# Kernel optimization log

Measured on AMD Instinct MI355X. Metric: run time of the kernel, lower is better.

## Reference

```python
import jax, jax.numpy as jnp
import numpy as np

B, T, D, H, K, V, L = 512, 80, 540, 6, 90, 30522, 6  # batch, ctx, d_model, heads, head_size, vocab, blocks


def _layernorm(x, g, b, eps=1e-5):
    m = jnp.mean(x, axis=-1, keepdims=True)
    v = jnp.mean(jnp.square(x - m), axis=-1, keepdims=True)
    return (x - m) * jax.lax.rsqrt(v + eps) * g + b


def setup_inputs() -> dict:
    key = jax.random.key(0)
    ks = jax.random.split(key, 12)
    s = 0.02
    return {
        "x_batch": jax.random.randint(ks[0], (B, T), 0, V),
        "embed": jax.random.normal(ks[1], (V, D), jnp.float32) * s,
        "pos_embed": jax.random.normal(ks[2], (T, D), jnp.float32) * s,
        # per-block stacked per-head projection weights, applied as x @ W
        "Wq": jax.random.normal(ks[3], (L, H, D, K), jnp.float32) * s,
        "Wk": jax.random.normal(ks[4], (L, H, D, K), jnp.float32) * s,
        "Wv": jax.random.normal(ks[5], (L, H, D, K), jnp.float32) * s,
        "W1": jax.random.normal(ks[6], (L, D, H * K), jnp.float32) * s,
        "b1": jnp.zeros((L, H * K), jnp.float32),
        "W2": jax.random.normal(ks[7], (L, H * K, D), jnp.float32) * s,
        "b2": jnp.zeros((L, D), jnp.float32),
        "ln1_g": jnp.ones((L, D), jnp.float32),
        "ln1_b": jnp.zeros((L, D), jnp.float32),
        "ln2_g": jnp.ones((L, D), jnp.float32),
        "ln2_b": jnp.zeros((L, D), jnp.float32),
        "Wc": jax.random.normal(ks[8], (T * D, 1), jnp.float32) * s,
        "bc": jnp.zeros((1,), jnp.float32),
    }


def reference(x_batch, embed, pos_embed, Wq, Wk, Wv, W1, b1, W2, b2,
              ln1_g, ln1_b, ln2_g, ln2_b, Wc, bc):
    x = embed[x_batch] + pos_embed[jnp.arange(x_batch.shape[1])]  # [B,T,D]
    scale = K ** -0.5
    for i in range(L):
        q = jnp.einsum('btd,hdk->bhtk', x, Wq[i])
        k = jnp.einsum('btd,hdk->bhtk', x, Wk[i])
        v = jnp.einsum('btd,hdk->bhtk', x, Wv[i])
        scores = jnp.einsum('btk,bsk->bts'.replace('b', 'bh'), q, k) * scale  # [B,H,T,T]
        # original: Softmax(dim=1) on [B,T,T] -> normalize over the QUERY axis
        attn = jax.nn.softmax(scores, axis=2)
        o = jnp.einsum('bhts,bhsk->bhtk', attn, v)
        o = o.transpose(0, 2, 1, 3).reshape(x.shape)  # concat heads -> [B,T,D]
        x = _layernorm(o + x, ln1_g[i], ln1_b[i])
        ff = jax.nn.relu(x @ W1[i] + b1[i]) @ W2[i] + b2[i]
        x = _layernorm(ff + x, ln2_g[i], ln2_b[i])
    flat = x.reshape(x.shape[0], -1)  # [B, T*D]
    return flat @ Wc + bc  # [B,1]
```

## Files before the change

kernel.cpp:

```cpp
#include <hip/hip_runtime.h>
#include <hip/hip_bf16.h>
#include <math.h>

typedef __hip_bfloat16 bf16;
typedef __bf16 bf16x8 __attribute__((ext_vector_type(8)));
typedef __bf16 bf16x4 __attribute__((ext_vector_type(4)));
typedef float floatx4 __attribute__((ext_vector_type(4)));

#define BB 512
#define TT 80
#define DD 540
#define HH 6
#define KK 90
#define LL 6
#define HK 540
#define KKA 96
#define HKA 576
#define NQA 1728
#define BT 40960
#define TD 43200
#define KP2 576
#define NQ2 1792
#define NF 640
#define NF2 768
#define TP 104
#define NKT2 18
#define BUFSZ 12288

__device__ inline float toF(bf16 x) { return __bfloat162float(x); }


__global__ void prep_wqkv(const float* __restrict__ Wq,
                          const float* __restrict__ Wk,
                          const float* __restrict__ Wv,
                          bf16* __restrict__ wTt) {
    int idx = blockIdx.x * blockDim.x + threadIdx.x;
    const int total = LL * NQ2 * KP2;
    if (idx >= total) return;
    int k = idx % KP2;
    int n = (idx / KP2) % NQ2;
    int l = idx / (KP2 * NQ2);
    float v = 0.f;
    if (k < DD && n < NQA) {
        int sel = n / HKA;
        int nn = n - sel * HKA;
        int h = nn / KKA, kk = nn - h * KKA;
        if (kk < KK) {
            const float* W = (sel == 0) ? Wq : ((sel == 1) ? Wk : Wv);
            v = W[(((size_t)l * HH + h) * DD + k) * KK + kk];
        }
    }
    wTt[idx] = __float2bfloat16(v);
}

__global__ void prep_wt(const float* __restrict__ W, bf16* __restrict__ Wt) {
    int idx = blockIdx.x * blockDim.x + threadIdx.x;
    const int total = LL * NF2 * KP2;
    if (idx >= total) return;
    int k = idx % KP2;
    int n = (idx / KP2) % NF2;
    int l = idx / (KP2 * NF2);
    float v = 0.f;
    if (k < DD && n < DD)
        v = W[((size_t)l * DD + k) * DD + n];
    Wt[idx] = __float2bfloat16(v);
}

__global__ void embed_kernel(const int* __restrict__ ids,
                             const float* __restrict__ embed,
                             const float* __restrict__ pos,
                             bf16* __restrict__ xc, int rows) {
    int idx = blockIdx.x * blockDim.x + threadIdx.x;
    int total = rows * KP2;
    if (idx >= total) return;
    int d = idx % KP2;
    int bt = idx / KP2;
    float v = 0.f;
    if (d < DD) {
        int t = bt % TT;
        v = embed[(size_t)ids[bt] * DD + d] + pos[t * DD + d];
    }
    xc[idx] = __float2bfloat16(v);
}


__device__ inline void stage3(const bf16* __restrict__ Ab, int lda,
                              const bf16* __restrict__ Bb,
                              bf16* ldsbuf, int k0, int tid) {
#pragma unroll
    for (int i = 0; i < 3; ++i) {
        int s = tid + i * 512;
        int isB = (s >= 512) ? 1 : 0;
        int s2 = s - isB * 512;
        int row = s2 >> 2, c = s2 & 3;
        int cs = c ^ ((row >> 1) & 3);
        const bf16* src = isB ? (Bb + (size_t)row * KP2 + k0 + cs * 8)
                              : (Ab + (size_t)row * lda + k0 + cs * 8);
        bf16* dst = ldsbuf + isB * 4096 + s2 * 8;
        __builtin_amdgcn_global_load_lds(
            (const __attribute__((address_space(1))) void*)src,
            (__attribute__((address_space(3))) void*)dst, 16, 0, 0);
    }
}

__global__ __launch_bounds__(512, 4) void mfma_gemm2(
    const bf16* __restrict__ A, int lda,
    const bf16* __restrict__ Bt,
    bf16* __restrict__ C, int ldc, int Nreal,
    const float* __restrict__ bias, int relu)
{
    extern __shared__ __align__(16) bf16 ldsb[];
    const int tid = threadIdx.x;
    const int lane = tid & 63;
    const int wave = tid >> 6;
    const int wr = wave >> 2;
    const int wc = wave & 3;
    const int q = lane >> 4, r = lane & 15;

    int bx = blockIdx.x, by = blockIdx.y;
    {
        int nwg = gridDim.x * gridDim.y;
        if ((nwg & 7) == 0) {
            int orig = by * gridDim.x + bx;
            int per = nwg >> 3;
            int swz = (orig & 7) * per + (orig >> 3);
            bx = swz % gridDim.x;
            by = swz / gridDim.x;
        }
    }
    const int row0 = by * 128;
    const int col0 = bx * 256;

    floatx4 acc[4][4];
#pragma unroll
    for (int i = 0; i < 4; ++i)
#pragma unroll
        for (int j = 0; j < 4; ++j) acc[i][j] = (floatx4){0.f, 0.f, 0.f, 0.f};

    const bf16* Ab = A + (size_t)row0 * lda;
    const bf16* Bb = Bt + (size_t)col0 * KP2;

    const int ksw = (q ^ ((r >> 1) & 3)) * 8;

    stage3(Ab, lda, Bb, ldsb, 0, tid);
    asm volatile("s_waitcnt vmcnt(0)" ::: "memory");
    __builtin_amdgcn_sched_barrier(0);
    __builtin_amdgcn_s_barrier();
    __builtin_amdgcn_sched_barrier(0);

    for (int kt = 0; kt < NKT2; ++kt) {
        bf16* buf  = ldsb + (kt & 1) * BUFSZ;
        bf16* sbuf = ldsb + ((kt + 1) & 1) * BUFSZ;

        if (kt + 1 < NKT2)
            stage3(Ab, lda, Bb, sbuf, (kt + 1) * 32, tid);

        bf16x8 a0[4], b0[4];
#pragma unroll
        for (int i = 0; i < 4; ++i) {
            int row_ = wr * 64 + i * 16 + r;
            a0[i] = *(const bf16x8*)(buf + row_ * 32 + ksw);
        }
#pragma unroll
        for (int j = 0; j < 4; ++j) {
            int row_ = wc * 64 + j * 16 + r;
            b0[j] = *(const bf16x8*)(buf + 4096 + row_ * 32 + ksw);
        }

        __builtin_amdgcn_s_setprio(1);
#pragma unroll
        for (int i = 0; i < 4; ++i)
#pragma unroll
            for (int j = 0; j < 4; ++j)
                acc[i][j] = __builtin_amdgcn_mfma_f32_16x16x32_bf16(
                    a0[i], b0[j], acc[i][j], 0, 0, 0);
        __builtin_amdgcn_s_setprio(0);

        asm volatile("s_waitcnt vmcnt(0)" ::: "memory");
        __builtin_amdgcn_sched_barrier(0);
        __builtin_amdgcn_s_barrier();
        __builtin_amdgcn_sched_barrier(0);
    }

#pragma unroll
    for (int mi = 0; mi < 4; ++mi) {
        int m0 = row0 + wr * 64 + mi * 16 + q * 4;
#pragma unroll
        for (int ni = 0; ni < 4; ++ni) {
            int n = col0 + wc * 64 + ni * 16 + r;
            if (n < ldc) {
                bool valid = (n < Nreal);
                float bv = (valid && bias) ? bias[n] : 0.f;
#pragma unroll
                for (int reg = 0; reg < 4; ++reg) {
                    float v = acc[mi][ni][reg] + bv;
                    if (relu) v = fmaxf(v, 0.f);
                    if (!valid) v = 0.f;
                    C[(size_t)(m0 + reg) * ldc + n] = __float2bfloat16(v);
                }
            }
        }
    }
}

__global__ __launch_bounds__(320) void attn_mfma(const bf16* __restrict__ qkv,
                                                 bf16* __restrict__ obuf) {
    extern __shared__ bf16 lds[];
    bf16* Qs = lds;
    bf16* Ks = lds + 80 * TP;
    bf16* Vt = lds + 160 * TP;
    __bf16* Vtb = (__bf16*)Vt;
    const int b = blockIdx.x / HH, h = blockIdx.x % HH;
    const int tid = threadIdx.x;
    const int lane = tid & 63;
    const int w = tid >> 6;
    const int q = lane >> 4, r = lane & 15;
    const bf16* base = qkv + (size_t)b * TT * NQA + h * KKA;

    for (int i = tid; i < TT * 12; i += 320) {
        int t = i / 12, kg = i % 12;
        const bf16* qr2 = base + (size_t)t * NQA + kg * 8;
        bf16x8 qv = *(const bf16x8*)qr2;
        bf16x8 kv2 = *(const bf16x8*)(qr2 + HKA);
        bf16x8 vv = *(const bf16x8*)(qr2 + 2 * HKA);
        *(bf16x8*)(Qs + t * TP + kg * 8) = qv;
        *(bf16x8*)(Ks + t * TP + kg * 8) = kv2;
#pragma unroll
        for (int j = 0; j < 8; ++j)
            Vtb[(kg * 8 + j) * TP + t] = vv[j];
    }
    for (int i = tid; i < 96 * 2; i += 320) {
        int kv = i >> 1, sg = i & 1;
        *(bf16x8*)(Vt + kv * TP + 80 + sg * 8) = (bf16x8)(__bf16)0.0f;
    }
    __syncthreads();

    floatx4 acc[5];
#pragma unroll
    for (int i = 0; i < 5; ++i) acc[i] = (floatx4){0.f, 0.f, 0.f, 0.f};
    bf16x8 bf[3];
#pragma unroll
    for (int ks = 0; ks < 3; ++ks)
        bf[ks] = *(const bf16x8*)(Ks + (16 * w + r) * TP + ks * 32 + q * 8);
#pragma unroll
    for (int ti = 0; ti < 5; ++ti) {
#pragma unroll
        for (int ks = 0; ks < 3; ++ks) {
            bf16x8 af = *(const bf16x8*)(Qs + (16 * ti + r) * TP + ks * 32 + q * 8);
            acc[ti] = __builtin_amdgcn_mfma_f32_16x16x32_bf16(af, bf[ks], acc[ti], 0, 0, 0);
        }
    }

    const float scale = 0.105409255338946f;
    float m = -1e30f;
#pragma unroll
    for (int ti = 0; ti < 5; ++ti)
#pragma unroll
        for (int reg = 0; reg < 4; ++reg) {
            acc[ti][reg] *= scale;
            m = fmaxf(m, acc[ti][reg]);
        }
    m = fmaxf(m, __shfl_xor(m, 16));
    m = fmaxf(m, __shfl_xor(m, 32));
    float sum = 0.f;
    float e[5][4];
#pragma unroll
    for (int ti = 0; ti < 5; ++ti)
#pragma unroll
        for (int reg = 0; reg < 4; ++reg) {
            e[ti][reg] = __expf(acc[ti][reg] - m);
            sum += e[ti][reg];
        }
    sum += __shfl_xor(sum, 16);
    sum += __shfl_xor(sum, 32);
    float inv = 1.f / sum;

    __syncthreads();

    bf16* P = Ks;
#pragma unroll
    for (int ti = 0; ti < 5; ++ti)
#pragma unroll
        for (int reg = 0; reg < 4; ++reg)
            P[(16 * ti + q * 4 + reg) * TP + 16 * w + r] =
                __float2bfloat16(e[ti][reg] * inv);
    for (int i = tid; i < TT * 2; i += 320) {
        int t2 = i >> 1, sg = i & 1;
        *(bf16x8*)(P + t2 * TP + 80 + sg * 8) = (bf16x8)(__bf16)0.0f;
    }
    __syncthreads();

    bf16x8 af2[3];
#pragma unroll
    for (int ks = 0; ks < 3; ++ks)
        af2[ks] = *(const bf16x8*)(P + (16 * w + r) * TP + ks * 32 + q * 8);
    bf16* ob = obuf + ((size_t)b * TT) * NF + h * KK;
#pragma unroll
    for (int nt = 0; nt < 6; ++nt) {
        floatx4 o = (floatx4){0.f, 0.f, 0.f, 0.f};
#pragma unroll
        for (int ks = 0; ks < 3; ++ks) {
            bf16x8 bv = *(const bf16x8*)(Vt + (16 * nt + r) * TP + ks * 32 + q * 8);
            o = __builtin_amdgcn_mfma_f32_16x16x32_bf16(af2[ks], bv, o, 0, 0, 0);
        }
        int kv = 16 * nt + r;
        if (kv < KK) {
#pragma unroll
            for (int reg = 0; reg < 4; ++reg) {
                int t2 = 16 * w + q * 4 + reg;
                ob[(size_t)t2 * NF + kv] = __float2bfloat16(o[reg]);
            }
        }
    }
}

__global__ __launch_bounds__(256) void add_ln_kernel(const bf16* __restrict__ delta,
                                                     bf16* __restrict__ x,
                                                     const float* __restrict__ g,
                                                     const float* __restrict__ bta,
                                                     int nrows) {
    const int w = threadIdx.x >> 6;
    const int lane = threadIdx.x & 63;
    const int row = blockIdx.x * 4 + w;
    if (row >= nrows) return;
    const bf16* dr = delta + (size_t)row * NF;
    bf16* xr = x + (size_t)row * KP2;

    float v[3][4];
    float s1 = 0.f, s2 = 0.f;
#pragma unroll
    for (int s = 0; s < 3; ++s) {
        int c = s * 256 + lane * 4;
        if (c < DD) {
            bf16x4 dv = *(const bf16x4*)(dr + c);
            bf16x4 xv = *(const bf16x4*)(xr + c);
#pragma unroll
            for (int j = 0; j < 4; ++j) {
                float t = (float)dv[j] + (float)xv[j];
                v[s][j] = t;
                s1 += t; s2 += t * t;
            }
        } else {
#pragma unroll
            for (int j = 0; j < 4; ++j) v[s][j] = 0.f;
        }
    }
#pragma unroll
    for (int o = 32; o > 0; o >>= 1) {
        s1 += __shfl_xor(s1, o, 64);
        s2 += __shfl_xor(s2, o, 64);
    }
    const float mean = s1 * (1.f / DD);
    const float var = s2 * (1.f / DD) - mean * mean;
    const float rstd = rsqrtf(var + 1e-5f);
#pragma unroll
    for (int s = 0; s < 3; ++s) {
        int c = s * 256 + lane * 4;
        if (c < DD) {
            float4 gv = *(const float4*)(g + c);
            float4 bv = *(const float4*)(bta + c);
            bf16x4 ov;
            ov[0] = (__bf16)((v[s][0] - mean) * rstd * gv.x + bv.x);
            ov[1] = (__bf16)((v[s][1] - mean) * rstd * gv.y + bv.y);
            ov[2] = (__bf16)((v[s][2] - mean) * rstd * gv.z + bv.z);
            ov[3] = (__bf16)((v[s][3] - mean) * rstd * gv.w + bv.w);
            *(bf16x4*)(xr + c) = ov;
        }
    }
}

__global__ __launch_bounds__(256) void final_kernel(const bf16* __restrict__ xc,
                                                    const float* __restrict__ Wc,
                                                    const float* __restrict__ bc,
                                                    float* __restrict__ out) {
    int b = blockIdx.x;
    int tid = threadIdx.x;
    const bf16* xb = xc + (size_t)b * TT * KP2;
    float s = 0.f;
    for (int i = tid; i < TD; i += 256) {
        int t = i / DD, d = i - t * DD;
        s += toF(xb[(size_t)t * KP2 + d]) * Wc[i];
    }
    for (int o = 32; o > 0; o >>= 1) s += __shfl_down(s, o, 64);
    __shared__ float red[4];
    int lane = tid & 63, w = tid >> 6;
    if (lane == 0) red[w] = s;
    __syncthreads();
    if (tid == 0) out[b] = red[0] + red[1] + red[2] + red[3] + bc[0];
}

extern "C" void kernel_launch(void* const* d_in, const int* in_sizes, int n_in,
                              void* d_out, int out_size, void* d_ws, size_t ws_size,
                              hipStream_t stream) {
    const int* ids    = (const int*)d_in[0];
    const float* embed = (const float*)d_in[1];
    const float* pos  = (const float*)d_in[2];
    const float* Wq   = (const float*)d_in[3];
    const float* Wk   = (const float*)d_in[4];
    const float* Wv   = (const float*)d_in[5];
    const float* W1   = (const float*)d_in[6];
    const float* b1   = (const float*)d_in[7];
    const float* W2   = (const float*)d_in[8];
    const float* b2   = (const float*)d_in[9];
    const float* ln1g = (const float*)d_in[10];
    const float* ln1b = (const float*)d_in[11];
    const float* ln2g = (const float*)d_in[12];
    const float* ln2b = (const float*)d_in[13];
    const float* Wc   = (const float*)d_in[14];
    const float* bc   = (const float*)d_in[15];
    float* out = (float*)d_out;

    const size_t wqkvB = (size_t)LL * NQ2 * KP2 * 2;
    const size_t wffB  = (size_t)LL * NF2 * KP2 * 2;
    const size_t fixed = wqkvB + 2 * wffB;
    const size_t perB  = (size_t)TT * 2 * (KP2 + NQA + NF);

    int bch = BB;
    while (bch > 16 && fixed + (size_t)bch * perB > ws_size) bch >>= 1;
    int nch = BB / bch;
    int rows = bch * TT;

    char* p = (char*)d_ws;
    bf16* wTt = (bf16*)p;  p += wqkvB;
    bf16* W1t = (bf16*)p;  p += wffB;
    bf16* W2t = (bf16*)p;  p += wffB;
    bf16* xc  = (bf16*)p;  p += (size_t)rows * KP2 * 2;
    bf16* scr = (bf16*)p;  p += (size_t)rows * NQA * 2;
    bf16* dch = (bf16*)p;

    prep_wqkv<<<(LL * NQ2 * KP2 + 255) / 256, 256, 0, stream>>>(Wq, Wk, Wv, wTt);
    prep_wt<<<(LL * NF2 * KP2 + 255) / 256, 256, 0, stream>>>(W1, W1t);
    prep_wt<<<(LL * NF2 * KP2 + 255) / 256, 256, 0, stream>>>(W2, W2t);

    dim3 gq(NQ2 / 256, rows / 128);
    dim3 gf(NF2 / 256, rows / 128);
    const size_t gemm_lds = 2 * BUFSZ * sizeof(bf16);
    const size_t attn_lds = (size_t)(160 + 96) * TP * 2;
    const int lnGrid = (rows + 3) / 4;

    for (int c = 0; c < nch; ++c) {
        embed_kernel<<<(rows * KP2 + 255) / 256, 256, 0, stream>>>(
            ids + (size_t)c * rows, embed, pos, xc, rows);
        for (int l = 0; l < LL; ++l) {
            mfma_gemm2<<<gq, 512, gemm_lds, stream>>>(
                xc, KP2, wTt + (size_t)l * NQ2 * KP2, scr, NQA, NQA,
                (const float*)nullptr, 0);
            attn_mfma<<<bch * HH, 320, attn_lds, stream>>>(scr, dch);
            add_ln_kernel<<<lnGrid, 256, 0, stream>>>(dch, xc, ln1g + l * DD, ln1b + l * DD, rows);
            mfma_gemm2<<<gf, 512, gemm_lds, stream>>>(
                xc, KP2, W1t + (size_t)l * NF2 * KP2, scr, NF, HK,
                b1 + (size_t)l * HK, 1);
            mfma_gemm2<<<gf, 512, gemm_lds, stream>>>(
                scr, NF, W2t + (size_t)l * NF2 * KP2, dch, NF, DD,
                b2 + (size_t)l * DD, 0);
            add_ln_kernel<<<lnGrid, 256, 0, stream>>>(dch, xc, ln2g + l * DD, ln2b + l * DD, rows);
        }
        final_kernel<<<bch, 256, 0, stream>>>(xc, Wc, bc, out + (size_t)c * bch);
    }
}
```

Measured before the change: 2.128 ms.

## Triple-buffer GEMM prefetch and use 128-wide N tiles for FFN GEMMs

The bf16 MFMA GEMM is templated on its N tile width and moves from double to triple buffering. Loads now run two k-steps ahead, with partial vmcnt waits so one stage stays in flight. The FFN GEMMs switch to 128-wide N tiles, padding N only to 640 instead of 768, which cuts wasted MFMA work and weight staging on padded columns. The costs are more LDS per block, which can lower occupancy, and a different wave layout for the 128-wide variant.

```diff
diff --git a/kernel.cpp b/kernel.cpp
--- a/kernel.cpp
+++ b/kernel.cpp
@@ -22,10 +22,8 @@
 #define KP2 576
 #define NQ2 1792
 #define NF 640
-#define NF2 768
 #define TP 104
 #define NKT2 18
-#define BUFSZ 12288
 
 __device__ inline float toF(bf16 x) { return __bfloat162float(x); }
 
@@ -55,11 +53,11 @@
 
 __global__ void prep_wt(const float* __restrict__ W, bf16* __restrict__ Wt) {
     int idx = blockIdx.x * blockDim.x + threadIdx.x;
-    const int total = LL * NF2 * KP2;
+    const int total = LL * NF * KP2;
     if (idx >= total) return;
     int k = idx % KP2;
-    int n = (idx / KP2) % NF2;
-    int l = idx / (KP2 * NF2);
+    int n = (idx / KP2) % NF;
+    int l = idx / (KP2 * NF);
     float v = 0.f;
     if (k < DD && n < DD)
         v = W[((size_t)l * DD + k) * DD + n];
@@ -84,11 +82,13 @@
 }
 
 
-__device__ inline void stage3(const bf16* __restrict__ Ab, int lda,
+template<int BN>
+__device__ inline void stageT(const bf16* __restrict__ Ab, int lda,
                               const bf16* __restrict__ Bb,
                               bf16* ldsbuf, int k0, int tid) {
-#pragma unroll
-    for (int i = 0; i < 3; ++i) {
+    constexpr int LPT = (128 + BN) / 128;
+#pragma unroll
+    for (int i = 0; i < LPT; ++i) {
         int s = tid + i * 512;
         int isB = (s >= 512) ? 1 : 0;
         int s2 = s - isB * 512;
@@ -103,18 +103,23 @@
     }
 }
 
+template<int BN>
 __global__ __launch_bounds__(512, 4) void mfma_gemm2(
     const bf16* __restrict__ A, int lda,
     const bf16* __restrict__ Bt,
     bf16* __restrict__ C, int ldc, int Nreal,
     const float* __restrict__ bias, int relu)
 {
+    constexpr int WCN = BN / 64;
+    constexpr int WM  = 8 / WCN;
+    constexpr int MR  = 128 / (WM * 16);
+    constexpr int BUFSZ_ = (128 + BN) * 32;
     extern __shared__ __align__(16) bf16 ldsb[];
     const int tid = threadIdx.x;
     const int lane = tid & 63;
     const int wave = tid >> 6;
-    const int wr = wave >> 2;
-    const int wc = wave & 3;
+    const int wr = wave / WCN;
+    const int wc = wave % WCN;
     const int q = lane >> 4, r = lane & 15;
 
     int bx = blockIdx.x, by = blockIdx.y;
@@ -129,11 +134,11 @@
         }
     }
     const int row0 = by * 128;
-    const int col0 = bx * 256;
-
-    floatx4 acc[4][4];
-#pragma unroll
-    for (int i = 0; i < 4; ++i)
+    const int col0 = bx * BN;
+
+    floatx4 acc[MR][4];
+#pragma unroll
+    for (int i = 0; i < MR; ++i)
 #pragma unroll
         for (int j = 0; j < 4; ++j) acc[i][j] = (floatx4){0.f, 0.f, 0.f, 0.f};
 
@@ -142,49 +147,59 @@
 
     const int ksw = (q ^ ((r >> 1) & 3)) * 8;
 
-    stage3(Ab, lda, Bb, ldsb, 0, tid);
-    asm volatile("s_waitcnt vmcnt(0)" ::: "memory");
+    bf16* bp0 = ldsb;
+    bf16* bp1 = ldsb + BUFSZ_;
+    bf16* bp2 = ldsb + 2 * BUFSZ_;
+
+    stageT<BN>(Ab, lda, Bb, bp0, 0, tid);
+    stageT<BN>(Ab, lda, Bb, bp1, 32, tid);
+    if constexpr (BN == 256) asm volatile("s_waitcnt vmcnt(3)" ::: "memory");
+    else                     asm volatile("s_waitcnt vmcnt(2)" ::: "memory");
     __builtin_amdgcn_sched_barrier(0);
     __builtin_amdgcn_s_barrier();
     __builtin_amdgcn_sched_barrier(0);
 
     for (int kt = 0; kt < NKT2; ++kt) {
-        bf16* buf  = ldsb + (kt & 1) * BUFSZ;
-        bf16* sbuf = ldsb + ((kt + 1) & 1) * BUFSZ;
-
-        if (kt + 1 < NKT2)
-            stage3(Ab, lda, Bb, sbuf, (kt + 1) * 32, tid);
-
-        bf16x8 a0[4], b0[4];
-#pragma unroll
-        for (int i = 0; i < 4; ++i) {
-            int row_ = wr * 64 + i * 16 + r;
-            a0[i] = *(const bf16x8*)(buf + row_ * 32 + ksw);
+        if (kt + 2 < NKT2)
+            stageT<BN>(Ab, lda, Bb, bp2, (kt + 2) * 32, tid);
+
+        bf16x8 a0[MR], b0[4];
+#pragma unroll
+        for (int i = 0; i < MR; ++i) {
+            int row_ = wr * (MR * 16) + i * 16 + r;
+            a0[i] = *(const bf16x8*)(bp0 + row_ * 32 + ksw);
         }
 #pragma unroll
         for (int j = 0; j < 4; ++j) {
             int row_ = wc * 64 + j * 16 + r;
-            b0[j] = *(const bf16x8*)(buf + 4096 + row_ * 32 + ksw);
+            b0[j] = *(const bf16x8*)(bp0 + 4096 + row_ * 32 + ksw);
         }
 
         __builtin_amdgcn_s_setprio(1);
 #pragma unroll
-        for (int i = 0; i < 4; ++i)
+        for (int i = 0; i < MR; ++i)
 #pragma unroll
             for (int j = 0; j < 4; ++j)
                 acc[i][j] = __builtin_amdgcn_mfma_f32_16x16x32_bf16(
                     a0[i], b0[j], acc[i][j], 0, 0, 0);
         __builtin_amdgcn_s_setprio(0);
 
-        asm volatile("s_waitcnt vmcnt(0)" ::: "memory");
+        if (kt + 2 < NKT2) {
+            if constexpr (BN == 256) asm volatile("s_waitcnt vmcnt(3)" ::: "memory");
+            else                     asm volatile("s_waitcnt vmcnt(2)" ::: "memory");
+        } else {
+            asm volatile("s_waitcnt vmcnt(0)" ::: "memory");
+        }
         __builtin_amdgcn_sched_barrier(0);
         __builtin_amdgcn_s_barrier();
         __builtin_amdgcn_sched_barrier(0);
-    }
-
-#pragma unroll
-    for (int mi = 0; mi < 4; ++mi) {
-        int m0 = row0 + wr * 64 + mi * 16 + q * 4;
+
+        bf16* t = bp0; bp0 = bp1; bp1 = bp2; bp2 = t;
+    }
+
+#pragma unroll
+    for (int mi = 0; mi < MR; ++mi) {
+        int m0 = row0 + wr * (MR * 16) + mi * 16 + q * 4;
 #pragma unroll
         for (int ni = 0; ni < 4; ++ni) {
             int n = col0 + wc * 64 + ni * 16 + r;
@@ -411,7 +426,7 @@
     float* out = (float*)d_out;
 
     const size_t wqkvB = (size_t)LL * NQ2 * KP2 * 2;
-    const size_t wffB  = (size_t)LL * NF2 * KP2 * 2;
+    const size_t wffB  = (size_t)LL * NF * KP2 * 2;
     const size_t fixed = wqkvB + 2 * wffB;
     const size_t perB  = (size_t)TT * 2 * (KP2 + NQA + NF);
 
@@ -429,12 +444,13 @@
     bf16* dch = (bf16*)p;
 
     prep_wqkv<<<(LL * NQ2 * KP2 + 255) / 256, 256, 0, stream>>>(Wq, Wk, Wv, wTt);
-    prep_wt<<<(LL * NF2 * KP2 + 255) / 256, 256, 0, stream>>>(W1, W1t);
-    prep_wt<<<(LL * NF2 * KP2 + 255) / 256, 256, 0, stream>>>(W2, W2t);
+    prep_wt<<<(LL * NF * KP2 + 255) / 256, 256, 0, stream>>>(W1, W1t);
+    prep_wt<<<(LL * NF * KP2 + 255) / 256, 256, 0, stream>>>(W2, W2t);
 
     dim3 gq(NQ2 / 256, rows / 128);
-    dim3 gf(NF2 / 256, rows / 128);
-    const size_t gemm_lds = 2 * BUFSZ * sizeof(bf16);
+    dim3 gf(NF / 128, rows / 128);
+    const size_t gemm_lds_q = 3 * (128 + 256) * 32 * sizeof(bf16);
+    const size_t gemm_lds_f = 3 * (128 + 128) * 32 * sizeof(bf16);
     const size_t attn_lds = (size_t)(160 + 96) * TP * 2;
     const int lnGrid = (rows + 3) / 4;
 
@@ -442,16 +458,16 @@
         embed_kernel<<<(rows * KP2 + 255) / 256, 256, 0, stream>>>(
             ids + (size_t)c * rows, embed, pos, xc, rows);
         for (int l = 0; l < LL; ++l) {
-            mfma_gemm2<<<gq, 512, gemm_lds, stream>>>(
+            mfma_gemm2<256><<<gq, 512, gemm_lds_q, stream>>>(
                 xc, KP2, wTt + (size_t)l * NQ2 * KP2, scr, NQA, NQA,
                 (const float*)nullptr, 0);
             attn_mfma<<<bch * HH, 320, attn_lds, stream>>>(scr, dch);
             add_ln_kernel<<<lnGrid, 256, 0, stream>>>(dch, xc, ln1g + l * DD, ln1b + l * DD, rows);
-            mfma_gemm2<<<gf, 512, gemm_lds, stream>>>(
-                xc, KP2, W1t + (size_t)l * NF2 * KP2, scr, NF, HK,
+            mfma_gemm2<128><<<gf, 512, gemm_lds_f, stream>>>(
+                xc, KP2, W1t + (size_t)l * NF * KP2, scr, NF, HK,
                 b1 + (size_t)l * HK, 1);
-            mfma_gemm2<<<gf, 512, gemm_lds, stream>>>(
-                scr, NF, W2t + (size_t)l * NF2 * KP2, dch, NF, DD,
+            mfma_gemm2<128><<<gf, 512, gemm_lds_f, stream>>>(
+                scr, NF, W2t + (size_t)l * NF * KP2, dch, NF, DD,
                 b2 + (size_t)l * DD, 0);
             add_ln_kernel<<<lnGrid, 256, 0, stream>>>(dch, xc, ln2g + l * DD, ln2b + l * DD, rows);
         }
```

Result: faster. 1.974 ms (-7.2%).
